# Kernel tuning notes

Hardware: AMD Instinct MI355X
Metric: run time of the kernel (lower is better)

## Reference

```python
import jax, jax.numpy as jnp
import numpy as np

B, TIMES, N, D = 8, 288, 207, 64
FEA_IN = 295  # 7 (day-of-week) + 288 (time-of-day)


def setup_inputs() -> dict:
    key = jax.random.key(0)
    k0, k1, k2, k3, k4 = jax.random.split(key, 5)
    TE = jax.random.randint(k0, (B, TIMES, N, 2), 0, 288, dtype=jnp.int32)
    s1 = 1.0 / np.sqrt(FEA_IN)
    s2 = 1.0 / np.sqrt(D)
    W1 = jax.random.normal(k1, (FEA_IN, D), dtype=jnp.float32) * s1
    b1 = jax.random.normal(k2, (D,), dtype=jnp.float32) * s1
    W2 = jax.random.normal(k3, (D, D), dtype=jnp.float32) * s2
    b2 = jax.random.normal(k4, (D,), dtype=jnp.float32) * s2
    return {"TE": TE, "W1": W1, "b1": b1, "W2": W2, "b2": b2, "T": 288}


def reference(TE, W1, b1, W2, b2, T):
    # TE: [B, Times, N, 2] int. Only node 0's time features are used.
    te = TE[:, :, 0, :]  # [B, Times, 2]
    dow = jax.nn.one_hot(te[..., 0] % 7, 7, dtype=W1.dtype)      # [B, Times, 7]
    tod = jax.nn.one_hot(te[..., 1] % 288, T, dtype=W1.dtype)    # [B, Times, T]
    x = jnp.concatenate([dow, tod], axis=-1)                      # [B, Times, 295]
    # FeedForward([295, D, D]): linear -> relu -> linear (no residual/LN)
    h = jax.nn.relu(jnp.einsum('btf,fd->btd', x, W1) + b1)
    out = jnp.einsum('btd,de->bte', h, W2) + b2                   # [B, Times, D]
    # The original repeats the 295-dim features over N before the MLP;
    # since the MLP acts per-feature-vector, broadcasting after is identical math.
    n = TE.shape[2]
    return jnp.broadcast_to(out[:, :, None, :], (out.shape[0], out.shape[1], n, out.shape[2]))
```

## Files before the change

### kernel.cpp

```cpp
#include <hip/hip_runtime.h>

#define B_     8
#define TIMES_ 288
#define NN_    207
#define D_     64

typedef float f4_t __attribute__((ext_vector_type(4)));

__global__ __launch_bounds__(256) void TemEmbedding_45672682225716_kernel(
    const int*   __restrict__ TE,
    const float* __restrict__ W1,
    const float* __restrict__ b1,
    const float* __restrict__ W2,
    const float* __restrict__ b2,
    float*       __restrict__ out)
{
    __shared__ float h[D_];
    __shared__ float row[D_];

    const int bt  = blockIdx.x;
    const int tid = threadIdx.x;

    const int2 te = *(const int2*)(TE + (long long)bt * (NN_ * 2));
    int dow = te.x % 7;   if (dow < 0) dow += 7;
    int tod = te.y % 288; if (tod < 0) tod += 288;

    if (tid < D_) {
        float v = W1[dow * D_ + tid] + W1[(7 + tod) * D_ + tid] + b1[tid];
        h[tid] = v > 0.0f ? v : 0.0f;
    }
    __syncthreads();

    if (tid < D_) {
        float acc = b2[tid];
        #pragma unroll
        for (int j = 0; j < D_; ++j) {
            acc = fmaf(h[j], W2[j * D_ + tid], acc);
        }
        row[tid] = acc;
    }
    __syncthreads();

    const f4_t val = ((const f4_t*)row)[tid & 15];

    f4_t* out4 = (f4_t*)(out + (long long)bt * (NN_ * D_));
    const int total4 = NN_ * (D_ / 4);
    for (int i = tid; i < total4; i += 256) {
        __builtin_nontemporal_store(val, &out4[i]);
    }
}

extern "C" void kernel_launch(void* const* d_in, const int* in_sizes, int n_in,
                              void* d_out, int out_size, void* d_ws, size_t ws_size,
                              hipStream_t stream) {
    const int*   TE = (const int*)  d_in[0];
    const float* W1 = (const float*)d_in[1];
    const float* b1 = (const float*)d_in[2];
    const float* W2 = (const float*)d_in[3];
    const float* b2 = (const float*)d_in[4];
    float* out = (float*)d_out;

    dim3 grid(B_ * TIMES_);
    dim3 block(256);
    TemEmbedding_45672682225716_kernel<<<grid, block, 0, stream>>>(TE, W1, b1, W2, b2, out);
}
```

Before: 27.57 us.

## Split into row-compute kernel and pure broadcast-store kernel via workspace

The fused kernel is replaced by two launches. The first computes each 64-wide MLP output row with four rows per block, using every thread, and writes them to a workspace. The second broadcasts each row across 207 nodes with plain (non-nontemporal) unrolled stores, so the store loop no longer waits behind the serial MLP work. The cost is an extra launch and a small workspace round-trip, and the nontemporal store hint is dropped. A fused fallback remains for when the workspace is too small.

```diff
diff --git a/kernel.cpp b/kernel.cpp
--- a/kernel.cpp
+++ b/kernel.cpp
@@ -4,50 +4,84 @@
 #define TIMES_ 288
 #define NN_    207
 #define D_     64
+#define BT_    (B_ * TIMES_)
 
 typedef float f4_t __attribute__((ext_vector_type(4)));
 
-__global__ __launch_bounds__(256) void TemEmbedding_45672682225716_kernel(
+__global__ __launch_bounds__(256) void tem_compute_rows(
     const int*   __restrict__ TE,
     const float* __restrict__ W1,
     const float* __restrict__ b1,
     const float* __restrict__ W2,
     const float* __restrict__ b2,
-    float*       __restrict__ out)
+    float*       __restrict__ ws)
 {
-    __shared__ float h[D_];
-    __shared__ float row[D_];
-
-    const int bt  = blockIdx.x;
-    const int tid = threadIdx.x;
+    __shared__ float h[4][D_];
+    const int tid  = threadIdx.x;
+    const int grp  = tid >> 6;
+    const int lane = tid & 63;
+    const int bt   = blockIdx.x * 4 + grp;
 
     const int2 te = *(const int2*)(TE + (long long)bt * (NN_ * 2));
     int dow = te.x % 7;   if (dow < 0) dow += 7;
     int tod = te.y % 288; if (tod < 0) tod += 288;
 
+    float v = W1[dow * D_ + lane] + W1[(7 + tod) * D_ + lane] + b1[lane];
+    h[grp][lane] = v > 0.0f ? v : 0.0f;
+    __syncthreads();
+
+    float acc = b2[lane];
+    #pragma unroll
+    for (int j = 0; j < D_; ++j) {
+        acc = fmaf(h[grp][j], W2[j * D_ + lane], acc);
+    }
+    ws[bt * D_ + lane] = acc;
+}
+
+__global__ __launch_bounds__(256) void tem_broadcast(
+    const float* __restrict__ ws,
+    float*       __restrict__ out)
+{
+    const int bt  = blockIdx.x;
+    const int tid = threadIdx.x;
+
+    const f4_t val = ((const f4_t*)ws)[bt * (D_ / 4) + (tid & 15)];
+
+    f4_t* out4 = (f4_t*)(out + (long long)bt * (NN_ * D_));
+    const int total4 = NN_ * (D_ / 4);
+    #pragma unroll 4
+    for (int i = tid; i < total4; i += 256) {
+        out4[i] = val;
+    }
+}
+
+__global__ __launch_bounds__(256) void tem_fused(
+    const int* __restrict__ TE, const float* __restrict__ W1,
+    const float* __restrict__ b1, const float* __restrict__ W2,
+    const float* __restrict__ b2, float* __restrict__ out)
+{
+    __shared__ float h[D_];
+    __shared__ float row[D_];
+    const int bt  = blockIdx.x;
+    const int tid = threadIdx.x;
+    const int2 te = *(const int2*)(TE + (long long)bt * (NN_ * 2));
+    int dow = te.x % 7;   if (dow < 0) dow += 7;
+    int tod = te.y % 288; if (tod < 0) tod += 288;
     if (tid < D_) {
         float v = W1[dow * D_ + tid] + W1[(7 + tod) * D_ + tid] + b1[tid];
         h[tid] = v > 0.0f ? v : 0.0f;
     }
     __syncthreads();
-
     if (tid < D_) {
         float acc = b2[tid];
         #pragma unroll
-        for (int j = 0; j < D_; ++j) {
-            acc = fmaf(h[j], W2[j * D_ + tid], acc);
-        }
+        for (int j = 0; j < D_; ++j) acc = fmaf(h[j], W2[j * D_ + tid], acc);
         row[tid] = acc;
     }
     __syncthreads();
-
     const f4_t val = ((const f4_t*)row)[tid & 15];
-
     f4_t* out4 = (f4_t*)(out + (long long)bt * (NN_ * D_));
-    const int total4 = NN_ * (D_ / 4);
-    for (int i = tid; i < total4; i += 256) {
-        __builtin_nontemporal_store(val, &out4[i]);
-    }
+    for (int i = tid; i < NN_ * (D_ / 4); i += 256) out4[i] = val;
 }
 
 extern "C" void kernel_launch(void* const* d_in, const int* in_sizes, int n_in,
@@ -60,7 +94,12 @@
     const float* b2 = (const float*)d_in[4];
     float* out = (float*)d_out;
 
-    dim3 grid(B_ * TIMES_);
-    dim3 block(256);
-    TemEmbedding_45672682225716_kernel<<<grid, block, 0, stream>>>(TE, W1, b1, W2, b2, out);
+    const size_t ws_needed = (size_t)BT_ * D_ * sizeof(float);
+    if (ws_size >= ws_needed) {
+        float* rows = (float*)d_ws;
+        tem_compute_rows<<<dim3(BT_ / 4), dim3(256), 0, stream>>>(TE, W1, b1, W2, b2, rows);
+        tem_broadcast  <<<dim3(BT_),     dim3(256), 0, stream>>>(rows, out);
+    } else {
+        tem_fused<<<dim3(BT_), dim3(256), 0, stream>>>(TE, W1, b1, W2, b2, out);
+    }
 }
```

Result: slower. 28.89 us (+4.8%).
